# Kernel optimization log

Measured on AMD Instinct MI355X. Metric: run time of the kernel, lower is better.

## Reference

```python
import jax, jax.numpy as jnp
import numpy as np

IN_DIM = 1024
OUT_DIM = 1024
L = 4
HIDDEN = 64
EMB_DIM = 2 + 2 * 2 * L  # 18
BATCH = 8192
W0 = 30.0


def make_embedded_coords():
    gy, gx = jnp.meshgrid(jnp.linspace(-1.0, 1.0, OUT_DIM), jnp.linspace(-1.0, 1.0, IN_DIM), indexing='ij')
    coords = jnp.stack([gy, gx], axis=-1).reshape(-1, 2)  # [rows*cols, 2]
    embeds = [coords]
    for i in range(L):
        freq = 2.0 ** i
        embeds.append(jnp.sin(freq * jnp.pi * coords))
        embeds.append(jnp.cos(freq * jnp.pi * coords))
    return jnp.concatenate(embeds, axis=-1)  # [rows*cols, 18]


def setup_inputs() -> dict:
    key = jax.random.key(0)
    ks = jax.random.split(key, 8)
    # init scales matching torch code
    u = lambda k, shape, b: jax.random.uniform(k, shape, jnp.float32, -b, b)
    W1 = u(ks[0], (HIDDEN, EMB_DIM), 1.0 / EMB_DIM)
    b1 = u(ks[1], (HIDDEN,), 1.0 / np.sqrt(EMB_DIM))
    s2 = np.sqrt(6.0 / HIDDEN) / W0
    W2 = u(ks[2], (HIDDEN, HIDDEN), s2)
    b2 = u(ks[3], (HIDDEN,), 1.0 / np.sqrt(HIDDEN))
    W3 = u(ks[4], (1, HIDDEN), s2)
    b3 = u(ks[5], (1,), 1.0 / np.sqrt(HIDDEN))
    x = jax.random.normal(ks[6], (BATCH, IN_DIM), jnp.float32)
    bias = jnp.zeros((OUT_DIM,), jnp.float32)
    return {
        'x': x,
        'embedded_coords': make_embedded_coords(),
        'W1': W1, 'b1': b1, 'W2': W2, 'b2': b2, 'W3': W3, 'b3': b3,
        'bias': bias,
    }


def reference(x, embedded_coords, W1, b1, W2, b2, W3, b3, bias):
    rows = bias.shape[0]
    cols = x.shape[-1]
    # tiny fully-fused hypernet MLP over rows*cols coordinate points
    h = jnp.sin(W0 * (embedded_coords @ W1.T + b1))  # [rows*cols, 64]
    h = jnp.sin(W0 * (h @ W2.T + b2))                # [rows*cols, 64]
    W = (h @ W3.T + b3).reshape(rows, cols)          # generated weight
    return x @ W.T + bias                            # [batch, out_dim]
```

## Files before the change

### kernel.cpp

```cpp
#include <hip/hip_runtime.h>
#include <hip/hip_bf16.h>


typedef __attribute__((ext_vector_type(8))) short bf16x8;
typedef __attribute__((ext_vector_type(4))) float f32x4;

#define SIN_SCALE 4.77464829275686f

__device__ __forceinline__ unsigned short f2bf(float f) {
    union { float f; unsigned u; } v; v.f = f;
    unsigned r = v.u + 0x7fffu + ((v.u >> 16) & 1u);
    return (unsigned short)(r >> 16);
}

__device__ __forceinline__ unsigned pktrunc(float a, float b) {
    union { float f; unsigned u; } x, y; x.f = a; y.f = b;
    return (x.u >> 16) | (y.u & 0xffff0000u);
}

__device__ __forceinline__ float sinrev(float x) {
    return __builtin_amdgcn_sinf(x);
}

template <int OFF>
__device__ __forceinline__ float swz_add(float v) {
    return v + __int_as_float(__builtin_amdgcn_ds_swizzle(__float_as_int(v), OFF));
}

__device__ __forceinline__ void async_ld16(const void* g, void* l) {
    __builtin_amdgcn_global_load_lds(
        (__attribute__((address_space(1))) void*)g,
        (__attribute__((address_space(3))) void*)l, 16, 0, 0);
}

__global__ __launch_bounds__(256) void cast_x_kernel(
        const float4* __restrict__ x, unsigned short* __restrict__ xb) {
    long i = (long)blockIdx.x * 256 + threadIdx.x;
    float4 v = x[i];
    ushort4 o;
    o.x = f2bf(v.x); o.y = f2bf(v.y); o.z = f2bf(v.z); o.w = f2bf(v.w);
    *(ushort4*)(xb + i * 4) = o;
}

__global__ __launch_bounds__(256) void siren_tables_kernel(
        const float* __restrict__ ec,
        const float* __restrict__ W1, const float* __restrict__ b1,
        float* __restrict__ Zrow, float* __restrict__ Zcol) {
    int idx = blockIdx.x * 256 + threadIdx.x;
    int j = idx & 63;
    int t = idx >> 6;
    const float* wr = W1 + j * 18;
    if (t < 1024) {
        const float* pe = ec + (long)t * 1024 * 18;
        float z = b1[j];
        #pragma unroll
        for (int i = 0; i < 18; ++i) z += wr[i] * pe[i];
        Zrow[t * 64 + j] = SIN_SCALE * z;
    } else {
        int c = t - 1024;
        const float* pe = ec + (long)c * 18;
        float z = 0.f;
        #pragma unroll
        for (int i = 0; i < 18; ++i) z += wr[i] * (pe[i] - ec[i]);
        Zcol[c * 64 + j] = SIN_SCALE * z;
    }
}

__global__ __launch_bounds__(256, 3) void siren_w_kernel(
        const float* __restrict__ Zrow, const float* __restrict__ Zcol,
        const float* __restrict__ W2, const float* __restrict__ b2,
        const float* __restrict__ W3, const float* __restrict__ b3,
        unsigned short* __restrict__ Wout) {
    int lane = threadIdx.x & 63;
    int wv   = threadIdx.x >> 6;
    int ln   = lane & 15;
    int kq   = lane >> 4;

    bf16x8 bfrag[2][4];
    #pragma unroll
    for (int kc = 0; kc < 2; ++kc)
        #pragma unroll
        for (int nt = 0; nt < 4; ++nt) {
            const float* src = W2 + (nt * 16 + ln) * 64 + kc * 32 + kq * 8;
            union { bf16x8 v; unsigned u[4]; } tmp;
            #pragma unroll
            for (int q = 0; q < 4; ++q)
                tmp.u[q] = pktrunc(SIN_SCALE * src[2*q], SIN_SCALE * src[2*q + 1]);
            bfrag[kc][nt] = tmp.v;
        }
    float b2v[4], w3v[4];
    #pragma unroll
    for (int nt = 0; nt < 4; ++nt) {
        b2v[nt] = SIN_SCALE * b2[nt * 16 + ln];
        w3v[nt] = W3[nt * 16 + ln];
    }
    float b3s = b3[0];

    int wid = blockIdx.x * 4 + wv;
    int r   = wid >> 2;
    int c0  = (wid & 3) * 256;

    const float* zrp = Zrow + (long)r * 64 + kq * 8;
    float zr0[8], zr1[8];
    #pragma unroll
    for (int j = 0; j < 8; ++j) { zr0[j] = zrp[j]; zr1[j] = zrp[32 + j]; }

    for (int it = 0; it < 8; ++it) {
        int ca = c0 + it * 32 + ln;
        const float* zca = Zcol + (long)ca * 64 + kq * 8;
        const float* zcb = zca + 16 * 64;

        float sa0[8], sa1[8], sb0[8], sb1[8];
        #pragma unroll
        for (int j = 0; j < 8; ++j) {
            sa0[j] = sinrev(zr0[j] + zca[j]);
            sa1[j] = sinrev(zr1[j] + zca[32 + j]);
            sb0[j] = sinrev(zr0[j] + zcb[j]);
            sb1[j] = sinrev(zr1[j] + zcb[32 + j]);
        }
        union { bf16x8 v; unsigned u[4]; } a0, a1, bb0, bb1;
        #pragma unroll
        for (int q = 0; q < 4; ++q) {
            a0.u[q]  = pktrunc(sa0[2*q], sa0[2*q + 1]);
            a1.u[q]  = pktrunc(sa1[2*q], sa1[2*q + 1]);
            bb0.u[q] = pktrunc(sb0[2*q], sb0[2*q + 1]);
            bb1.u[q] = pktrunc(sb1[2*q], sb1[2*q + 1]);
        }

        f32x4 acca[4] = {}, accb[4] = {};
        #pragma unroll
        for (int nt = 0; nt < 4; ++nt) {
            acca[nt] = __builtin_amdgcn_mfma_f32_16x16x32_bf16(a0.v,  bfrag[0][nt], acca[nt], 0, 0, 0);
            accb[nt] = __builtin_amdgcn_mfma_f32_16x16x32_bf16(bb0.v, bfrag[0][nt], accb[nt], 0, 0, 0);
            acca[nt] = __builtin_amdgcn_mfma_f32_16x16x32_bf16(a1.v,  bfrag[1][nt], acca[nt], 0, 0, 0);
            accb[nt] = __builtin_amdgcn_mfma_f32_16x16x32_bf16(bb1.v, bfrag[1][nt], accb[nt], 0, 0, 0);
        }

        float pa[4], pb[4];
        #pragma unroll
        for (int rg = 0; rg < 4; ++rg) {
            float s = 0.f, t2 = 0.f;
            #pragma unroll
            for (int nt = 0; nt < 4; ++nt) {
                s  += w3v[nt] * sinrev(acca[nt][rg] + b2v[nt]);
                t2 += w3v[nt] * sinrev(accb[nt][rg] + b2v[nt]);
            }
            pa[rg] = s; pb[rg] = t2;
        }
        #pragma unroll
        for (int rg = 0; rg < 4; ++rg) {
            pa[rg] = swz_add<0x041F>(pa[rg]);  pb[rg] = swz_add<0x041F>(pb[rg]);
            pa[rg] = swz_add<0x081F>(pa[rg]);  pb[rg] = swz_add<0x081F>(pb[rg]);
            pa[rg] = swz_add<0x101F>(pa[rg]);  pb[rg] = swz_add<0x101F>(pb[rg]);
            pa[rg] = swz_add<0x201F>(pa[rg]);  pb[rg] = swz_add<0x201F>(pb[rg]);
        }

        if (ln == 0) {
            long p0 = (long)r * 1024 + c0 + it * 32;
            ushort4 oa, ob;
            oa.x = f2bf(pa[0] + b3s); oa.y = f2bf(pa[1] + b3s);
            oa.z = f2bf(pa[2] + b3s); oa.w = f2bf(pa[3] + b3s);
            ob.x = f2bf(pb[0] + b3s); ob.y = f2bf(pb[1] + b3s);
            ob.z = f2bf(pb[2] + b3s); ob.w = f2bf(pb[3] + b3s);
            *(ushort4*)(Wout + p0 + kq * 4)      = oa;
            *(ushort4*)(Wout + p0 + 16 + kq * 4) = ob;
        }
    }
}

__global__ __launch_bounds__(256) void gemm_kernel(
        const unsigned short* __restrict__ A,
        const unsigned short* __restrict__ B,
        const float* __restrict__ bias,
        float* __restrict__ C) {
    const int K = 1024;
    __shared__ __align__(16) unsigned short As[128 * 32];
    __shared__ __align__(16) unsigned short Bs[128 * 32];

    int tid  = threadIdx.x;
    int lane = tid & 63;
    int wv   = tid >> 6;
    int wm   = wv & 1, wn = wv >> 1;
    long Abase = (long)blockIdx.x * 128 * K;
    long Bbase = (long)blockIdx.y * 128 * K;

    int sr = tid >> 2;
    int sc = tid & 3;
    int rsel = lane & 15;
    int csel = lane >> 4;

    f32x4 acc[4][4] = {};

    for (int kt = 0; kt < K; kt += 32) {
        #pragma unroll
        for (int q = 0; q < 2; ++q) {
            int row = q * 64 + sr;
            int cc  = sc ^ ((row >> 1) & 3);
            const unsigned short* ga = A + Abase + (long)row * K + kt + cc * 8;
            const unsigned short* gb = B + Bbase + (long)row * K + kt + cc * 8;
            unsigned short* la = &As[(q * 256 + wv * 64) * 8];
            unsigned short* lb = &Bs[(q * 256 + wv * 64) * 8];
            async_ld16(ga, la);
            async_ld16(gb, lb);
        }
        __syncthreads();

        bf16x8 af[4], bf[4];
        #pragma unroll
        for (int mi = 0; mi < 4; ++mi) {
            int row = wm * 64 + mi * 16 + rsel;
            int ch  = csel ^ ((row >> 1) & 3);
            af[mi] = *(const bf16x8*)&As[row * 32 + ch * 8];
        }
        #pragma unroll
        for (int ni = 0; ni < 4; ++ni) {
            int row = wn * 64 + ni * 16 + rsel;
            int ch  = csel ^ ((row >> 1) & 3);
            bf[ni] = *(const bf16x8*)&Bs[row * 32 + ch * 8];
        }
        #pragma unroll
        for (int mi = 0; mi < 4; ++mi)
            #pragma unroll
            for (int ni = 0; ni < 4; ++ni)
                acc[mi][ni] = __builtin_amdgcn_mfma_f32_16x16x32_bf16(
                    af[mi], bf[ni], acc[mi][ni], 0, 0, 0);
        __syncthreads();
    }

    int row0 = blockIdx.x * 128 + wm * 64;
    int col0 = blockIdx.y * 128 + wn * 64;
    #pragma unroll
    for (int ni = 0; ni < 4; ++ni) {
        int col = col0 + ni * 16 + rsel;
        float bv = bias[col];
        #pragma unroll
        for (int mi = 0; mi < 4; ++mi) {
            int rbase = row0 + mi * 16 + csel * 4;
            #pragma unroll
            for (int r = 0; r < 4; ++r)
                C[(long)(rbase + r) * 1024 + col] = acc[mi][ni][r] + bv;
        }
    }
}

extern "C" void kernel_launch(void* const* d_in, const int* in_sizes, int n_in,
                              void* d_out, int out_size, void* d_ws, size_t ws_size,
                              hipStream_t stream) {
    const float* x    = (const float*)d_in[0];
    const float* ec   = (const float*)d_in[1];
    const float* W1   = (const float*)d_in[2];
    const float* b1   = (const float*)d_in[3];
    const float* W2   = (const float*)d_in[4];
    const float* b2   = (const float*)d_in[5];
    const float* W3   = (const float*)d_in[6];
    const float* b3   = (const float*)d_in[7];
    const float* bias = (const float*)d_in[8];
    float* out = (float*)d_out;

    unsigned short* xb = (unsigned short*)d_ws;
    unsigned short* Wb = xb + (size_t)8192 * 1024;
    float* Zrow = (float*)(Wb + (size_t)1024 * 1024);
    float* Zcol = Zrow + 1024 * 64;

    cast_x_kernel<<<8192, 256, 0, stream>>>((const float4*)x, xb);
    siren_tables_kernel<<<512, 256, 0, stream>>>(ec, W1, b1, Zrow, Zcol);
    siren_w_kernel<<<1024, 256, 0, stream>>>(Zrow, Zcol, W2, b2, W3, b3, Wb);
    dim3 g(64, 8);
    gemm_kernel<<<g, 256, 0, stream>>>(xb, Wb, bias, out);
}
```

Before: 209.6 us.

## Merge cast and table kernels; double GEMM K-tile to 64 with 8-way swizzle

The x-to-bf16 cast and the first-layer table kernels are merged into one launch, removing a kernel launch and its gap. The GEMM K-step per iteration grows from 32 to 64, with shared tiles doubled and the LDS swizzle changed to XOR over 8 chunks. This halves the number of barrier pairs and load rounds per tile and gives more MFMA work between syncs. The cost is more LDS per block, which may lower occupancy.

```diff
diff --git a/kernel.cpp b/kernel.cpp
--- a/kernel.cpp
+++ b/kernel.cpp
@@ -33,36 +33,37 @@
         (__attribute__((address_space(3))) void*)l, 16, 0, 0);
 }
 
-__global__ __launch_bounds__(256) void cast_x_kernel(
-        const float4* __restrict__ x, unsigned short* __restrict__ xb) {
-    long i = (long)blockIdx.x * 256 + threadIdx.x;
-    float4 v = x[i];
-    ushort4 o;
-    o.x = f2bf(v.x); o.y = f2bf(v.y); o.z = f2bf(v.z); o.w = f2bf(v.w);
-    *(ushort4*)(xb + i * 4) = o;
-}
-
-__global__ __launch_bounds__(256) void siren_tables_kernel(
+__global__ __launch_bounds__(256) void prep_kernel(
+        const float4* __restrict__ x, unsigned short* __restrict__ xb,
         const float* __restrict__ ec,
         const float* __restrict__ W1, const float* __restrict__ b1,
         float* __restrict__ Zrow, float* __restrict__ Zcol) {
-    int idx = blockIdx.x * 256 + threadIdx.x;
-    int j = idx & 63;
-    int t = idx >> 6;
-    const float* wr = W1 + j * 18;
-    if (t < 1024) {
-        const float* pe = ec + (long)t * 1024 * 18;
-        float z = b1[j];
-        #pragma unroll
-        for (int i = 0; i < 18; ++i) z += wr[i] * pe[i];
-        Zrow[t * 64 + j] = SIN_SCALE * z;
+    int b = blockIdx.x;
+    if (b < 8192) {
+        long i = (long)b * 256 + threadIdx.x;
+        float4 v = x[i];
+        ushort4 o;
+        o.x = f2bf(v.x); o.y = f2bf(v.y); o.z = f2bf(v.z); o.w = f2bf(v.w);
+        *(ushort4*)(xb + i * 4) = o;
     } else {
-        int c = t - 1024;
-        const float* pe = ec + (long)c * 18;
-        float z = 0.f;
-        #pragma unroll
-        for (int i = 0; i < 18; ++i) z += wr[i] * (pe[i] - ec[i]);
-        Zcol[c * 64 + j] = SIN_SCALE * z;
+        int idx = (b - 8192) * 256 + threadIdx.x;
+        int j = idx & 63;
+        int t = idx >> 6;
+        const float* wr = W1 + j * 18;
+        if (t < 1024) {
+            const float* pe = ec + (long)t * 1024 * 18;
+            float z = b1[j];
+            #pragma unroll
+            for (int i = 0; i < 18; ++i) z += wr[i] * pe[i];
+            Zrow[t * 64 + j] = SIN_SCALE * z;
+        } else {
+            int c = t - 1024;
+            const float* pe = ec + (long)c * 18;
+            float z = 0.f;
+            #pragma unroll
+            for (int i = 0; i < 18; ++i) z += wr[i] * (pe[i] - ec[i]);
+            Zcol[c * 64 + j] = SIN_SCALE * z;
+        }
     }
 }
 
@@ -174,8 +175,8 @@
         const float* __restrict__ bias,
         float* __restrict__ C) {
     const int K = 1024;
-    __shared__ __align__(16) unsigned short As[128 * 32];
-    __shared__ __align__(16) unsigned short Bs[128 * 32];
+    __shared__ __align__(16) unsigned short As[128 * 64];
+    __shared__ __align__(16) unsigned short Bs[128 * 64];
 
     int tid  = threadIdx.x;
     int lane = tid & 63;
@@ -184,18 +185,18 @@
     long Abase = (long)blockIdx.x * 128 * K;
     long Bbase = (long)blockIdx.y * 128 * K;
 
-    int sr = tid >> 2;
-    int sc = tid & 3;
+    int sr8 = tid >> 3;
+    int sl  = tid & 7;
     int rsel = lane & 15;
-    int csel = lane >> 4;
+    int kq   = lane >> 4;
 
     f32x4 acc[4][4] = {};
 
-    for (int kt = 0; kt < K; kt += 32) {
-        #pragma unroll
-        for (int q = 0; q < 2; ++q) {
-            int row = q * 64 + sr;
-            int cc  = sc ^ ((row >> 1) & 3);
+    for (int kt = 0; kt < K; kt += 64) {
+        #pragma unroll
+        for (int q = 0; q < 4; ++q) {
+            int row = q * 32 + sr8;
+            int cc  = sl ^ (row & 7);
             const unsigned short* ga = A + Abase + (long)row * K + kt + cc * 8;
             const unsigned short* gb = B + Bbase + (long)row * K + kt + cc * 8;
             unsigned short* la = &As[(q * 256 + wv * 64) * 8];
@@ -205,25 +206,28 @@
         }
         __syncthreads();
 
-        bf16x8 af[4], bf[4];
-        #pragma unroll
-        for (int mi = 0; mi < 4; ++mi) {
-            int row = wm * 64 + mi * 16 + rsel;
-            int ch  = csel ^ ((row >> 1) & 3);
-            af[mi] = *(const bf16x8*)&As[row * 32 + ch * 8];
-        }
-        #pragma unroll
-        for (int ni = 0; ni < 4; ++ni) {
-            int row = wn * 64 + ni * 16 + rsel;
-            int ch  = csel ^ ((row >> 1) & 3);
-            bf[ni] = *(const bf16x8*)&Bs[row * 32 + ch * 8];
-        }
-        #pragma unroll
-        for (int mi = 0; mi < 4; ++mi)
-            #pragma unroll
-            for (int ni = 0; ni < 4; ++ni)
-                acc[mi][ni] = __builtin_amdgcn_mfma_f32_16x16x32_bf16(
-                    af[mi], bf[ni], acc[mi][ni], 0, 0, 0);
+        #pragma unroll
+        for (int h = 0; h < 2; ++h) {
+            bf16x8 af[4], bf[4];
+            #pragma unroll
+            for (int mi = 0; mi < 4; ++mi) {
+                int row = wm * 64 + mi * 16 + rsel;
+                int ch  = (h * 4 + kq) ^ (row & 7);
+                af[mi] = *(const bf16x8*)&As[row * 64 + ch * 8];
+            }
+            #pragma unroll
+            for (int ni = 0; ni < 4; ++ni) {
+                int row = wn * 64 + ni * 16 + rsel;
+                int ch  = (h * 4 + kq) ^ (row & 7);
+                bf[ni] = *(const bf16x8*)&Bs[row * 64 + ch * 8];
+            }
+            #pragma unroll
+            for (int mi = 0; mi < 4; ++mi)
+                #pragma unroll
+                for (int ni = 0; ni < 4; ++ni)
+                    acc[mi][ni] = __builtin_amdgcn_mfma_f32_16x16x32_bf16(
+                        af[mi], bf[ni], acc[mi][ni], 0, 0, 0);
+        }
         __syncthreads();
     }
 
@@ -235,7 +239,7 @@
         float bv = bias[col];
         #pragma unroll
         for (int mi = 0; mi < 4; ++mi) {
-            int rbase = row0 + mi * 16 + csel * 4;
+            int rbase = row0 + mi * 16 + kq * 4;
             #pragma unroll
             for (int r = 0; r < 4; ++r)
                 C[(long)(rbase + r) * 1024 + col] = acc[mi][ni][r] + bv;
@@ -262,8 +266,7 @@
     float* Zrow = (float*)(Wb + (size_t)1024 * 1024);
     float* Zcol = Zrow + 1024 * 64;
 
-    cast_x_kernel<<<8192, 256, 0, stream>>>((const float4*)x, xb);
-    siren_tables_kernel<<<512, 256, 0, stream>>>(ec, W1, b1, Zrow, Zcol);
+    prep_kernel<<<8704, 256, 0, stream>>>((const float4*)x, xb, ec, W1, b1, Zrow, Zcol);
     siren_w_kernel<<<1024, 256, 0, stream>>>(Zrow, Zcol, W2, b2, W3, b3, Wb);
     dim3 g(64, 8);
     gemm_kernel<<<g, 256, 0, stream>>>(xb, Wb, bias, out);
```

Result: no change. 206.8 us (-1.3%).
